# Performance work log

Hardware: AMD Instinct MI355X
Metric: run time of the kernel (lower is better)

Reference implementation:

```python
import jax, jax.numpy as jnp
import numpy as np

# Constants from the source's eval path
BBOX_STDS = (0.1, 0.1, 0.2, 0.2)   # cfg.TRAIN.BBOX_NORMALIZE_STDS (MEANS are zeros)
PRE_NMS = 300                       # cfg.TEST.RPN_POST_NMS_TOP_N
POST_K = 100                        # cfg.PERSON_NMS (fixed output size; zero-padded)
NMS_THRESH = 0.3
SCORE_THRESH = 0.05


def setup_inputs() -> dict:
    key = jax.random.key(0)
    k1, k2, k3, k4 = jax.random.split(key, 4)
    B, N = 64, 32768
    H = W = 1024.0
    # plausible RPN proposal boxes inside the image
    xy = jax.random.uniform(k1, (B, N, 2)) * (W - 160.0)
    wh = jax.random.uniform(k2, (B, N, 2)) * 120.0 + 8.0
    boxes = jnp.concatenate([xy, xy + wh], axis=-1)          # [B,N,4] x1y1x2y2
    cls_prob = jax.random.uniform(k3, (B, N, 2))              # softmax probs [bg, person]
    box_deltas = jax.random.normal(k4, (B, N, 4)) * 0.5
    im_info = jnp.tile(jnp.array([H, W, 1.0], jnp.float32), (B, 1))
    return {"cls_prob": cls_prob, "boxes": boxes, "box_deltas": box_deltas, "im_info": im_info}


def _decode_and_clip(boxes, deltas, im_info):
    # bbox_transform_inv with de-normalized deltas, then clip_boxes
    stds = jnp.array(BBOX_STDS, boxes.dtype)
    d = deltas * stds                                         # MEANS are zero
    w = boxes[..., 2] - boxes[..., 0] + 1.0
    h = boxes[..., 3] - boxes[..., 1] + 1.0
    cx = boxes[..., 0] + 0.5 * w
    cy = boxes[..., 1] + 0.5 * h
    pcx = d[..., 0] * w + cx
    pcy = d[..., 1] * h + cy
    pw = jnp.exp(d[..., 2]) * w
    ph = jnp.exp(d[..., 3]) * h
    x1 = pcx - 0.5 * pw
    y1 = pcy - 0.5 * ph
    x2 = pcx + 0.5 * pw
    y2 = pcy + 0.5 * ph
    hmax = im_info[:, 0][:, None] - 1.0   # [B,1]
    wmax = im_info[:, 1][:, None] - 1.0
    x1 = jnp.clip(x1, 0.0, wmax)
    y1 = jnp.clip(y1, 0.0, hmax)
    x2 = jnp.clip(x2, 0.0, wmax)
    y2 = jnp.clip(y2, 0.0, hmax)
    return jnp.stack([x1, y1, x2, y2], axis=-1)               # [B,N,4]


def _nms_single(boxes_i, scores_i):
    # threshold -> sort (top-k) -> greedy NMS -> fixed-size padded output
    valid = scores_i >= SCORE_THRESH
    s = jnp.where(valid, scores_i, -jnp.inf)
    topv, topi = jax.lax.top_k(s, PRE_NMS)                    # descending sort + pre_nms_topN
    b = boxes_i[topi]                                          # [M,4]
    x1, y1, x2, y2 = b[:, 0], b[:, 1], b[:, 2], b[:, 3]
    areas = (x2 - x1 + 1.0) * (y2 - y1 + 1.0)
    xx1 = jnp.maximum(x1[:, None], x1[None, :])
    yy1 = jnp.maximum(y1[:, None], y1[None, :])
    xx2 = jnp.minimum(x2[:, None], x2[None, :])
    yy2 = jnp.minimum(y2[:, None], y2[None, :])
    inter = jnp.maximum(xx2 - xx1 + 1.0, 0.0) * jnp.maximum(yy2 - yy1 + 1.0, 0.0)
    iou = inter / (areas[:, None] + areas[None, :] - inter)    # [M,M]
    iou = jax.lax.stop_gradient(iou)                           # only drives the boolean keep mask
    idx = jnp.arange(PRE_NMS)
    keep0 = jnp.isfinite(topv)                                 # drop below-threshold padding

    def body(i, keep):
        sup = (iou[i] > NMS_THRESH) & (idx > i) & keep[i]
        return keep & ~sup

    keep = jax.lax.fori_loop(0, PRE_NMS, body, keep0)
    # compact kept boxes (in score order) into a fixed [POST_K,4] buffer, zero-padded
    rank = jnp.cumsum(keep) - 1
    dst = jnp.where(keep & (rank < POST_K), rank, POST_K)      # overflow row POST_K is discarded
    out = jnp.zeros((POST_K + 1, 4), b.dtype).at[dst].set(b)
    return out[:POST_K]


def reference(cls_prob, boxes, box_deltas, im_info):
    pred = _decode_and_clip(boxes, box_deltas, im_info)        # [B,N,4]
    scores_person = cls_prob[:, :, 1]                          # person column
    kept = jax.vmap(_nms_single)(pred, scores_person)          # [B,POST_K,4]
    B = pred.shape[0]
    bidx = jnp.broadcast_to(jnp.arange(B, dtype=pred.dtype)[:, None, None], (B, POST_K, 1))
    return jnp.concatenate([bidx, kept], axis=-1)              # [B,POST_K,5] rois
```

## Files before the change

kernel.cpp:

```cpp
#include <hip/hip_runtime.h>
#include <cstdint>
#include <cstddef>

#define PRE_NMS  300
#define POST_K   100
#define NBUCKET  4096
#define CAND_MAX 2048
#define NCHUNK   16
#define SUB      128
#define NWORDS   5
#define SUP_STRIDE 8
#define NBUK     512
#define MBASE    0xC0800000u
#define NMS_T    0.3f
#define SCORE_T  0.05f
#define FAST_T   0.9875f

typedef unsigned long long u64;

__global__ __launch_bounds__(256) void scan_kernel(
    const float* __restrict__ cls_prob,
    u64* __restrict__ candG,
    int* __restrict__ cntG,
    int N)
{
    const int b     = blockIdx.x >> 4;
    const int chunk = blockIdx.x & (NCHUNK - 1);
    const int nq    = N / 2;
    const int per   = (nq + NCHUNK - 1) / NCHUNK;
    const int base  = chunk * per;
    const int end   = min(base + per, nq);

    __shared__ int lcnt;
    __shared__ u64 lbuf[SUB];
    if (threadIdx.x == 0) lcnt = 0;
    __syncthreads();

    const float4* cp = (const float4*)(cls_prob + (size_t)b * N * 2);
    for (int q = base + threadIdx.x; q < end; q += 256) {
        float4 v = cp[q];
        #pragma unroll
        for (int h = 0; h < 2; ++h) {
            float s = h ? v.w : v.y;
            if (s >= FAST_T) {
                int pos = atomicAdd(&lcnt, 1);
                if (pos < SUB) {
                    unsigned int m = __float_as_uint(s) ^ 0xFFFFFFFFu;
                    lbuf[pos] = ((u64)m << 32) | (unsigned int)(2 * q + h);
                }
            }
        }
    }
    __syncthreads();

    const int cnt = lcnt;
    u64* cb = candG + ((size_t)b * NCHUNK + chunk) * SUB;
    for (int i = threadIdx.x; i < min(cnt, SUB); i += 256) cb[i] = lbuf[i];
    if (threadIdx.x == 0) cntG[b * NCHUNK + chunk] = cnt;
}

__device__ __forceinline__ u64 keep_init_word(int Kv, int w) {
    int rem = Kv - 64 * w;
    if (rem >= 64) return ~0ull;
    if (rem <= 0)  return 0ull;
    return (1ull << rem) - 1ull;
}

__device__ __forceinline__ u64 bits_above(int b) {
    return (b == 63) ? 0ull : (~0ull << (b + 1));
}

__device__ __forceinline__ int key_bucket(u64 key) {
    unsigned int m = (unsigned int)(key >> 32);
    int d = (int)(m - MBASE);
    if (d < 0) return 0;
    int bu = d >> 9;
    return (bu > NBUK - 1) ? (NBUK - 1) : bu;
}

__global__ __launch_bounds__(512) void proposal_kernel(
    const float* __restrict__ cls_prob,
    const float* __restrict__ boxes,
    const float* __restrict__ deltas,
    const float* __restrict__ im_info,
    float* __restrict__ out,
    const u64* __restrict__ candG,
    const int* __restrict__ cntG,
    int useWS, int N)
{
    const int b   = blockIdx.x;
    const int tid = threadIdx.x;
    const int NT  = 512;

    __shared__ u64 cand[CAND_MAX];
    int* hist4k = (int*)cand;
    __shared__ float4 bb[PRE_NMS];
    int* buk_off = (int*)bb;
    int* buk_cnt = buk_off + NBUK;
    __shared__ u64 supRow[PRE_NMS * SUP_STRIDE];
    u64* skey2 = supRow;
    __shared__ u64 skey[PRE_NMS];
    __shared__ u64 keepw[NWORDS];
    __shared__ int sel[POST_K];
    __shared__ int ws8[8];
    __shared__ int n_out;
    __shared__ int sh_cc;
    __shared__ int sh_ok;
    __shared__ int cand_count;
    __shared__ int cutoff;
    __shared__ int ccnt[NCHUNK], coff[NCHUNK + 1];

    if (tid == 0) cand_count = 0;
    __syncthreads();

    const float4* cp = (const float4*)(cls_prob + (size_t)b * N * 2);
    const int nq = N / 2;

    if (useWS && tid < NCHUNK) ccnt[tid] = cntG[b * NCHUNK + tid];
    __syncthreads();
    if (tid == 0) {
        int ok = useWS;
        int tot = 0;
        if (useWS) {
            for (int c = 0; c < NCHUNK; ++c) {
                if (ccnt[c] > SUB) ok = 0;
                coff[c] = tot;
                tot += ccnt[c];
            }
            coff[NCHUNK] = tot;
            if (tot < PRE_NMS || tot > CAND_MAX) ok = 0;
        }
        sh_ok = ok;
        sh_cc = tot;
    }
    __syncthreads();
    const bool fast = (sh_ok != 0);
    int cc;

    if (fast) {
        cc = sh_cc;
        const int c = tid >> 5;
        const u64* cb = candG + ((size_t)b * NCHUNK + c) * SUB;
        const int n = ccnt[c], o = coff[c];
        for (int i = tid & 31; i < n; i += 32) cand[o + i] = cb[i];
        __syncthreads();

        for (int i = tid; i < NBUK; i += NT) { buk_off[i] = 0; buk_cnt[i] = 0; }
        __syncthreads();
        for (int c2 = tid; c2 < cc; c2 += NT)
            atomicAdd(&buk_off[key_bucket(cand[c2])], 1);
        __syncthreads();
        {
            int v = buk_off[tid];
            int lane = tid & 63;
            int incl = v;
            #pragma unroll
            for (int d = 1; d < 64; d <<= 1) {
                int nv = __shfl_up(incl, d, 64);
                if (lane >= d) incl += nv;
            }
            if (lane == 63) ws8[tid >> 6] = incl;
            __syncthreads();
            int woff = 0;
            #pragma unroll
            for (int w = 0; w < 8; ++w)
                if (w < (tid >> 6)) woff += ws8[w];
            __syncthreads();
            buk_off[tid] = woff + incl - v;
        }
        __syncthreads();
        for (int c2 = tid; c2 < cc; c2 += NT) {
            u64 my = cand[c2];
            int bu = key_bucket(my);
            int slot = buk_off[bu] + atomicAdd(&buk_cnt[bu], 1);
            skey2[slot] = my;
        }
        __syncthreads();
        for (int s = tid; s < cc; s += NT) {
            u64 my = skey2[s];
            int bu = key_bucket(my);
            int o = buk_off[bu], n = buk_cnt[bu];
            int r = o;
            for (int t = o; t < o + n; ++t) r += (skey2[t] < my) ? 1 : 0;
            if (r < PRE_NMS) skey[r] = my;
        }
        __syncthreads();
    } else {
        for (int q = tid; q < nq; q += NT) {
            float4 v = cp[q];
            #pragma unroll
            for (int h = 0; h < 2; ++h) {
                float s = h ? v.w : v.y;
                if (s >= FAST_T) {
                    int pos = atomicAdd(&cand_count, 1);
                    if (pos < CAND_MAX) {
                        unsigned int m = __float_as_uint(s) ^ 0xFFFFFFFFu;
                        cand[pos] = ((u64)m << 32) | (unsigned int)(2 * q + h);
                    }
                }
            }
        }
        __syncthreads();
        if (cand_count < PRE_NMS) {
            for (int i = tid; i < NBUCKET; i += NT) hist4k[i] = 0;
            __syncthreads();
            for (int q = tid; q < nq; q += NT) {
                float4 v = cp[q];
                if (v.y >= SCORE_T) atomicAdd(&hist4k[min((int)(v.y * (float)NBUCKET), NBUCKET - 1)], 1);
                if (v.w >= SCORE_T) atomicAdd(&hist4k[min((int)(v.w * (float)NBUCKET), NBUCKET - 1)], 1);
            }
            __syncthreads();
            if (tid == 0) {
                int acc = 0, c = 0;
                for (int i = NBUCKET - 1; i >= 0; --i) {
                    acc += hist4k[i];
                    if (acc >= PRE_NMS) { c = i; break; }
                }
                cutoff = c;
                cand_count = 0;
            }
            __syncthreads();
            const int c = cutoff;
            for (int q = tid; q < nq; q += NT) {
                float4 v = cp[q];
                #pragma unroll
                for (int h = 0; h < 2; ++h) {
                    float s = h ? v.w : v.y;
                    if (s >= SCORE_T) {
                        int bu = min((int)(s * (float)NBUCKET), NBUCKET - 1);
                        if (bu >= c) {
                            int pos = atomicAdd(&cand_count, 1);
                            if (pos < CAND_MAX) {
                                unsigned int m = __float_as_uint(s) ^ 0xFFFFFFFFu;
                                cand[pos] = ((u64)m << 32) | (unsigned int)(2 * q + h);
                            }
                        }
                    }
                }
            }
            __syncthreads();
        }
        cc = min(cand_count, CAND_MAX);
        if (tid == 0) sh_cc = cc;
        __syncthreads();
        cc = sh_cc;
        for (int c2 = tid; c2 < cc; c2 += NT) {
            u64 my = cand[c2];
            int r = 0;
            for (int k = 0; k < cc; ++k) r += (cand[k] < my) ? 1 : 0;
            if (r < PRE_NMS) skey[r] = my;
        }
        __syncthreads();
    }

    const int Kv = min(cc, PRE_NMS);

    const float hmax = im_info[b * 3 + 0] - 1.0f;
    const float wmax = im_info[b * 3 + 1] - 1.0f;
    if (tid < PRE_NMS) {
        if (tid < Kv) {
            int idx = (int)(skey[tid] & 0xFFFFFFFFull);
            float4 bo = *(const float4*)(boxes  + ((size_t)b * N + idx) * 4);
            float4 de = *(const float4*)(deltas + ((size_t)b * N + idx) * 4);
            float w  = bo.z - bo.x + 1.0f;
            float hh = bo.w - bo.y + 1.0f;
            float cx = bo.x + 0.5f * w;
            float cy = bo.y + 0.5f * hh;
            float pcx = de.x * 0.1f * w + cx;
            float pcy = de.y * 0.1f * hh + cy;
            float pw  = expf(de.z * 0.2f) * w;
            float ph  = expf(de.w * 0.2f) * hh;
            float x1 = fminf(fmaxf(pcx - 0.5f * pw, 0.0f), wmax);
            float y1 = fminf(fmaxf(pcy - 0.5f * ph, 0.0f), hmax);
            float x2 = fminf(fmaxf(pcx + 0.5f * pw, 0.0f), wmax);
            float y2 = fminf(fmaxf(pcy + 0.5f * ph, 0.0f), hmax);
            bb[tid] = make_float4(x1, y1, x2, y2);
        } else {
            bb[tid] = make_float4(0.f, 0.f, 0.f, 0.f);
        }
    }
    __syncthreads();

    {
        const int lane = tid & 63;
        const int wv   = tid >> 6;
        float4 cb[5]; float ca[5];
        #pragma unroll
        for (int g = 0; g < 5; ++g) {
            int j = g * 64 + lane;
            float4 v = bb[(j < PRE_NMS) ? j : (PRE_NMS - 1)];
            cb[g] = v;
            ca[g] = (v.z - v.x + 1.0f) * (v.w - v.y + 1.0f);
        }
        for (int i = wv; i < PRE_NMS; i += 8) {
            float4 bi = bb[i];
            float ai = (bi.z - bi.x + 1.0f) * (bi.w - bi.y + 1.0f);
            const int wi = i >> 6, bbit = i & 63;
            u64* rp = supRow + (size_t)i * SUP_STRIDE;
            #pragma unroll
            for (int g = 0; g < 5; ++g) {
                u64 word = 0;
                if (g >= wi) {
                    int j = g * 64 + lane;
                    float xx1 = fmaxf(bi.x, cb[g].x);
                    float yy1 = fmaxf(bi.y, cb[g].y);
                    float xx2 = fminf(bi.z, cb[g].z);
                    float yy2 = fminf(bi.w, cb[g].w);
                    float iw = fmaxf(xx2 - xx1 + 1.0f, 0.0f);
                    float ih = fmaxf(yy2 - yy1 + 1.0f, 0.0f);
                    float inter = iw * ih;
                    bool ov = (inter > NMS_T * (ai + ca[g] - inter)) && (j < PRE_NMS);
                    u64 bal = __ballot(ov);
                    word = (g == wi) ? (bal & bits_above(bbit)) : bal;
                }
                if (lane == 0) rp[g] = word;
            }
        }
    }
    __syncthreads();

    if (tid < 64) {
        u64 kw0 = keep_init_word(Kv, 0);
        u64 kw1 = keep_init_word(Kv, 1);
        u64 kw2 = keep_init_word(Kv, 2);
        u64 kw3 = keep_init_word(Kv, 3);
        u64 kw4 = keep_init_word(Kv, 4);

        int nk = 0;
        #pragma unroll
        for (int wi = 0; wi < NWORDS; ++wi) {
            if (nk >= POST_K) break;
            u64 w = (wi == 0) ? kw0 : (wi == 1) ? kw1 : (wi == 2) ? kw2 : (wi == 3) ? kw3 : kw4;
            while (w != 0ull && nk < POST_K) {
                int b1 = __ffsll(w) - 1;
                u64 w1 = w & bits_above(b1);
                int b2 = (w1 != 0ull) ? (__ffsll(w1) - 1) : -1;
                u64 w2 = (b2 >= 0) ? (w1 & bits_above(b2)) : 0ull;
                int b3 = (w2 != 0ull) ? (__ffsll(w2) - 1) : -1;
                u64 w3 = (b3 >= 0) ? (w2 & bits_above(b3)) : 0ull;
                int b4 = (w3 != 0ull) ? (__ffsll(w3) - 1) : -1;

                const int base = wi * 64;
                const u64* p1 = supRow + (size_t)(base + b1) * SUP_STRIDE;
                const u64* p2 = supRow + (size_t)(base + ((b2 >= 0) ? b2 : b1)) * SUP_STRIDE;
                const u64* p3 = supRow + (size_t)(base + ((b3 >= 0) ? b3 : b1)) * SUP_STRIDE;
                const u64* p4 = supRow + (size_t)(base + ((b4 >= 0) ? b4 : b1)) * SUP_STRIDE;
                u64 a0 = p1[0], a1 = p1[1], a2 = p1[2], a3 = p1[3], a4 = p1[4];
                u64 c0 = p2[0], c1 = p2[1], c2 = p2[2], c3 = p2[3], c4 = p2[4];
                u64 d0 = p3[0], d1 = p3[1], d2 = p3[2], d3 = p3[3], d4 = p3[4];
                u64 e0 = p4[0], e1 = p4[1], e2 = p4[2], e3 = p4[3], e4 = p4[4];

                u64 aw = (wi == 0) ? a0 : (wi == 1) ? a1 : (wi == 2) ? a2 : (wi == 3) ? a3 : a4;
                u64 cw = (wi == 0) ? c0 : (wi == 1) ? c1 : (wi == 2) ? c2 : (wi == 3) ? c3 : c4;
                u64 dw = (wi == 0) ? d0 : (wi == 1) ? d1 : (wi == 2) ? d2 : (wi == 3) ? d3 : d4;

                kw0 &= ~a0; kw1 &= ~a1; kw2 &= ~a2; kw3 &= ~a3; kw4 &= ~a4;
                ++nk;
                bool k2 = false, k3 = false;
                if (b2 >= 0 && nk < POST_K && !((aw >> b2) & 1ull)) {
                    kw0 &= ~c0; kw1 &= ~c1; kw2 &= ~c2; kw3 &= ~c3; kw4 &= ~c4;
                    ++nk; k2 = true;
                }
                if (b3 >= 0 && nk < POST_K && !((aw >> b3) & 1ull)
                    && !(k2 && ((cw >> b3) & 1ull))) {
                    kw0 &= ~d0; kw1 &= ~d1; kw2 &= ~d2; kw3 &= ~d3; kw4 &= ~d4;
                    ++nk; k3 = true;
                }
                if (b4 >= 0 && nk < POST_K && !((aw >> b4) & 1ull)
                    && !(k2 && ((cw >> b4) & 1ull))
                    && !(k3 && ((dw >> b4) & 1ull))) {
                    kw0 &= ~e0; kw1 &= ~e1; kw2 &= ~e2; kw3 &= ~e3; kw4 &= ~e4;
                    ++nk;
                }
                int blast = (b4 >= 0) ? b4 : ((b3 >= 0) ? b3 : ((b2 >= 0) ? b2 : b1));
                u64 self = (wi == 0) ? kw0 : (wi == 1) ? kw1 : (wi == 2) ? kw2 : (wi == 3) ? kw3 : kw4;
                w = self & bits_above(blast);
            }
        }
        if (tid == 0) {
            keepw[0] = kw0; keepw[1] = kw1; keepw[2] = kw2; keepw[3] = kw3; keepw[4] = kw4;
            n_out = nk;
        }
    }
    __syncthreads();

    if (tid < PRE_NMS) {
        int wi = tid >> 6, bi = tid & 63;
        u64 w = keepw[wi];
        int prefix = 0;
        #pragma unroll
        for (int ww = 0; ww < NWORDS; ++ww)
            if (ww < wi) prefix += __popcll(keepw[ww]);
        prefix += __popcll(w & ((1ull << bi) - 1ull));
        if (((w >> bi) & 1ull) && prefix < POST_K) sel[prefix] = tid;
    }
    __syncthreads();

    if (tid < POST_K) {
        float* op = out + ((size_t)b * POST_K + tid) * 5;
        op[0] = (float)b;
        if (tid < n_out) {
            float4 v = bb[sel[tid]];
            op[1] = v.x; op[2] = v.y; op[3] = v.z; op[4] = v.w;
        } else {
            op[1] = 0.0f; op[2] = 0.0f; op[3] = 0.0f; op[4] = 0.0f;
        }
    }
}

extern "C" void kernel_launch(void* const* d_in, const int* in_sizes, int n_in,
                              void* d_out, int out_size, void* d_ws, size_t ws_size,
                              hipStream_t stream) {
    const float* cls_prob = (const float*)d_in[0];
    const float* boxes    = (const float*)d_in[1];
    const float* deltas   = (const float*)d_in[2];
    const float* im_info  = (const float*)d_in[3];
    float* out = (float*)d_out;

    const int B = in_sizes[3] / 3;
    const int N = in_sizes[0] / (B * 2);

    int* cntG   = (int*)d_ws;
    u64* candG  = (u64*)((char*)d_ws + 16384);
    size_t need = 16384 + (size_t)B * NCHUNK * SUB * sizeof(u64);
    int useWS   = (ws_size >= need && B * NCHUNK * (int)sizeof(int) <= 16384) ? 1 : 0;

    if (useWS) {
        scan_kernel<<<B * NCHUNK, 256, 0, stream>>>(cls_prob, candG, cntG, N);
    }
    proposal_kernel<<<B, 512, 0, stream>>>(cls_prob, boxes, deltas, im_info, out,
                                           candG, cntG, useWS, N);
}
```

Measured before the change: 134.3 us.

## Restrict NMS suppression matrix to top 192 candidates with full fallback

```diff
diff --git a/kernel.cpp b/kernel.cpp
--- a/kernel.cpp
+++ b/kernel.cpp
@@ -9,6 +9,8 @@
 #define NCHUNK   16
 #define SUB      128
 #define NWORDS   5
+#define KCAP     192
+#define KW       3
 #define SUP_STRIDE 8
 #define NBUK     512
 #define MBASE    0xC0800000u
@@ -76,6 +78,10 @@
     if (d < 0) return 0;
     int bu = d >> 9;
     return (bu > NBUK - 1) ? (NBUK - 1) : bu;
+}
+
+__device__ __forceinline__ float box_area(float4 v) {
+    return (v.z - v.x + 1.0f) * (v.w - v.y + 1.0f);
 }
 
 __global__ __launch_bounds__(512) void proposal_kernel(
@@ -104,13 +110,14 @@
     __shared__ int sel[POST_K];
     __shared__ int ws8[8];
     __shared__ int n_out;
+    __shared__ int need_full;
     __shared__ int sh_cc;
     __shared__ int sh_ok;
     __shared__ int cand_count;
     __shared__ int cutoff;
     __shared__ int ccnt[NCHUNK], coff[NCHUNK + 1];
 
-    if (tid == 0) cand_count = 0;
+    if (tid == 0) { cand_count = 0; need_full = 0; }
     __syncthreads();
 
     const float4* cp = (const float4*)(cls_prob + (size_t)b * N * 2);
@@ -284,24 +291,22 @@
     {
         const int lane = tid & 63;
         const int wv   = tid >> 6;
-        float4 cb[5]; float ca[5];
+        float4 cb[KW]; float ca[KW];
         #pragma unroll
-        for (int g = 0; g < 5; ++g) {
-            int j = g * 64 + lane;
-            float4 v = bb[(j < PRE_NMS) ? j : (PRE_NMS - 1)];
+        for (int g = 0; g < KW; ++g) {
+            float4 v = bb[g * 64 + lane];
             cb[g] = v;
-            ca[g] = (v.z - v.x + 1.0f) * (v.w - v.y + 1.0f);
-        }
-        for (int i = wv; i < PRE_NMS; i += 8) {
+            ca[g] = box_area(v);
+        }
+        for (int i = wv; i < KCAP; i += 8) {
             float4 bi = bb[i];
-            float ai = (bi.z - bi.x + 1.0f) * (bi.w - bi.y + 1.0f);
+            float ai = box_area(bi);
             const int wi = i >> 6, bbit = i & 63;
             u64* rp = supRow + (size_t)i * SUP_STRIDE;
             #pragma unroll
-            for (int g = 0; g < 5; ++g) {
+            for (int g = 0; g < KW; ++g) {
                 u64 word = 0;
                 if (g >= wi) {
-                    int j = g * 64 + lane;
                     float xx1 = fmaxf(bi.x, cb[g].x);
                     float yy1 = fmaxf(bi.y, cb[g].y);
                     float xx2 = fminf(bi.z, cb[g].z);
@@ -309,7 +314,7 @@
                     float iw = fmaxf(xx2 - xx1 + 1.0f, 0.0f);
                     float ih = fmaxf(yy2 - yy1 + 1.0f, 0.0f);
                     float inter = iw * ih;
-                    bool ov = (inter > NMS_T * (ai + ca[g] - inter)) && (j < PRE_NMS);
+                    bool ov = (inter > NMS_T * (ai + ca[g] - inter));
                     u64 bal = __ballot(ov);
                     word = (g == wi) ? (bal & bits_above(bbit)) : bal;
                 }
@@ -323,14 +328,12 @@
         u64 kw0 = keep_init_word(Kv, 0);
         u64 kw1 = keep_init_word(Kv, 1);
         u64 kw2 = keep_init_word(Kv, 2);
-        u64 kw3 = keep_init_word(Kv, 3);
-        u64 kw4 = keep_init_word(Kv, 4);
 
         int nk = 0;
         #pragma unroll
-        for (int wi = 0; wi < NWORDS; ++wi) {
+        for (int wi = 0; wi < KW; ++wi) {
             if (nk >= POST_K) break;
-            u64 w = (wi == 0) ? kw0 : (wi == 1) ? kw1 : (wi == 2) ? kw2 : (wi == 3) ? kw3 : kw4;
+            u64 w = (wi == 0) ? kw0 : (wi == 1) ? kw1 : kw2;
             while (w != 0ull && nk < POST_K) {
                 int b1 = __ffsll(w) - 1;
                 u64 w1 = w & bits_above(b1);
@@ -345,44 +348,93 @@
                 const u64* p2 = supRow + (size_t)(base + ((b2 >= 0) ? b2 : b1)) * SUP_STRIDE;
                 const u64* p3 = supRow + (size_t)(base + ((b3 >= 0) ? b3 : b1)) * SUP_STRIDE;
                 const u64* p4 = supRow + (size_t)(base + ((b4 >= 0) ? b4 : b1)) * SUP_STRIDE;
-                u64 a0 = p1[0], a1 = p1[1], a2 = p1[2], a3 = p1[3], a4 = p1[4];
-                u64 c0 = p2[0], c1 = p2[1], c2 = p2[2], c3 = p2[3], c4 = p2[4];
-                u64 d0 = p3[0], d1 = p3[1], d2 = p3[2], d3 = p3[3], d4 = p3[4];
-                u64 e0 = p4[0], e1 = p4[1], e2 = p4[2], e3 = p4[3], e4 = p4[4];
-
-                u64 aw = (wi == 0) ? a0 : (wi == 1) ? a1 : (wi == 2) ? a2 : (wi == 3) ? a3 : a4;
-                u64 cw = (wi == 0) ? c0 : (wi == 1) ? c1 : (wi == 2) ? c2 : (wi == 3) ? c3 : c4;
-                u64 dw = (wi == 0) ? d0 : (wi == 1) ? d1 : (wi == 2) ? d2 : (wi == 3) ? d3 : d4;
-
-                kw0 &= ~a0; kw1 &= ~a1; kw2 &= ~a2; kw3 &= ~a3; kw4 &= ~a4;
+                u64 a0 = p1[0], a1 = p1[1], a2 = p1[2];
+                u64 c0 = p2[0], c1 = p2[1], c2 = p2[2];
+                u64 d0 = p3[0], d1 = p3[1], d2 = p3[2];
+                u64 e0 = p4[0], e1 = p4[1], e2 = p4[2];
+
+                u64 aw = (wi == 0) ? a0 : (wi == 1) ? a1 : a2;
+                u64 cw = (wi == 0) ? c0 : (wi == 1) ? c1 : c2;
+                u64 dw = (wi == 0) ? d0 : (wi == 1) ? d1 : d2;
+
+                kw0 &= ~a0; kw1 &= ~a1; kw2 &= ~a2;
                 ++nk;
                 bool k2 = false, k3 = false;
                 if (b2 >= 0 && nk < POST_K && !((aw >> b2) & 1ull)) {
-                    kw0 &= ~c0; kw1 &= ~c1; kw2 &= ~c2; kw3 &= ~c3; kw4 &= ~c4;
+                    kw0 &= ~c0; kw1 &= ~c1; kw2 &= ~c2;
                     ++nk; k2 = true;
                 }
                 if (b3 >= 0 && nk < POST_K && !((aw >> b3) & 1ull)
                     && !(k2 && ((cw >> b3) & 1ull))) {
-                    kw0 &= ~d0; kw1 &= ~d1; kw2 &= ~d2; kw3 &= ~d3; kw4 &= ~d4;
+                    kw0 &= ~d0; kw1 &= ~d1; kw2 &= ~d2;
                     ++nk; k3 = true;
                 }
                 if (b4 >= 0 && nk < POST_K && !((aw >> b4) & 1ull)
                     && !(k2 && ((cw >> b4) & 1ull))
                     && !(k3 && ((dw >> b4) & 1ull))) {
-                    kw0 &= ~e0; kw1 &= ~e1; kw2 &= ~e2; kw3 &= ~e3; kw4 &= ~e4;
+                    kw0 &= ~e0; kw1 &= ~e1; kw2 &= ~e2;
                     ++nk;
                 }
                 int blast = (b4 >= 0) ? b4 : ((b3 >= 0) ? b3 : ((b2 >= 0) ? b2 : b1));
-                u64 self = (wi == 0) ? kw0 : (wi == 1) ? kw1 : (wi == 2) ? kw2 : (wi == 3) ? kw3 : kw4;
+                u64 self = (wi == 0) ? kw0 : (wi == 1) ? kw1 : kw2;
                 w = self & bits_above(blast);
             }
         }
         if (tid == 0) {
-            keepw[0] = kw0; keepw[1] = kw1; keepw[2] = kw2; keepw[3] = kw3; keepw[4] = kw4;
+            keepw[0] = kw0; keepw[1] = kw1; keepw[2] = kw2;
+            keepw[3] = 0ull; keepw[4] = 0ull;
             n_out = nk;
-        }
-    }
-    __syncthreads();
+            need_full = (nk < POST_K && Kv > KCAP) ? 1 : 0;
+        }
+    }
+    __syncthreads();
+
+    if (need_full) {
+        for (int t = tid; t < PRE_NMS * NWORDS; t += NT) {
+            int w = t / PRE_NMS;
+            int i = t - w * PRE_NMS;
+            int jbase = w * 64;
+            int jend  = min(jbase + 64, PRE_NMS);
+            u64 bits = 0;
+            int jstart = max(jbase, i + 1);
+            if (jstart < jend) {
+                float4 bi = bb[i];
+                float ai = box_area(bi);
+                for (int j = jstart; j < jend; ++j) {
+                    float4 bj = bb[j];
+                    float aj = box_area(bj);
+                    float xx1 = fmaxf(bi.x, bj.x);
+                    float yy1 = fmaxf(bi.y, bj.y);
+                    float xx2 = fminf(bi.z, bj.z);
+                    float yy2 = fminf(bi.w, bj.w);
+                    float iw = fmaxf(xx2 - xx1 + 1.0f, 0.0f);
+                    float ih = fmaxf(yy2 - yy1 + 1.0f, 0.0f);
+                    float inter = iw * ih;
+                    if (inter > NMS_T * (ai + aj - inter)) bits |= (1ull << (j - jbase));
+                }
+            }
+            supRow[i * SUP_STRIDE + w] = bits;
+        }
+        __syncthreads();
+        if (tid == 0) {
+            u64 kk[NWORDS];
+            #pragma unroll
+            for (int w = 0; w < NWORDS; ++w) kk[w] = keep_init_word(Kv, w);
+            int nk = 0;
+            for (int i = 0; i < PRE_NMS && nk < POST_K; ++i) {
+                if ((kk[i >> 6] >> (i & 63)) & 1ull) {
+                    const u64* r = supRow + (size_t)i * SUP_STRIDE;
+                    #pragma unroll
+                    for (int w = 0; w < NWORDS; ++w) kk[w] &= ~r[w];
+                    ++nk;
+                }
+            }
+            #pragma unroll
+            for (int w = 0; w < NWORDS; ++w) keepw[w] = kk[w];
+            n_out = nk;
+        }
+        __syncthreads();
+    }
 
     if (tid < PRE_NMS) {
         int wi = tid >> 6, bi = tid & 63;
```

Result: faster. 125.2 us (-6.8%).
